# Optimization experiments

Hardware: AMD Instinct MI355X
Metric: run time of the kernel (lower is better)

The kernel has to match this reference:

```python
import jax, jax.numpy as jnp
import numpy as np

T, B, D, H, E = 16, 4096, 256, 512, 32
EPS = 0.1

def setup_inputs() -> dict:
    key = jax.random.key(0)
    ks = jax.random.split(key, 8)
    return {
        "term_emb": jax.random.normal(ks[0], (T, B, D), dtype=jnp.float32),
        "pred_emb": jax.random.normal(ks[1], (E, B, D), dtype=jnp.float32),
        "inv_pred_emb": jax.random.normal(ks[2], (E, B, D), dtype=jnp.float32),
        "signs": jnp.ones((E,), dtype=jnp.float32),
        "W1": jax.random.normal(ks[3], (D, H), dtype=jnp.float32) * (1.0 / np.sqrt(D)),
        "b1": jnp.zeros((H,), dtype=jnp.float32),
        "W2": jax.random.normal(ks[4], (H, D), dtype=jnp.float32) * (1.0 / np.sqrt(H)),
        "b2": jnp.zeros((D,), dtype=jnp.float32),
        "heads": jax.random.randint(ks[5], (E,), 0, T, dtype=jnp.int64),
        "tails": jax.random.randint(ks[6], (E,), 0, T, dtype=jnp.int64),
    }

def reference(term_emb, pred_emb, inv_pred_emb, signs, W1, b1, W2, b2, heads, tails):
    # gather endpoint embeddings per edge: [E, B, D]
    h = term_emb[heads]
    t = term_emb[tails]
    s = signs[:, None, None]
    # estimate_tail_emb (TransE-style NBP): translate by relation embedding
    msg_to_tail = s * (h + pred_emb)      # message along edge direction
    msg_to_head = s * (t + inv_pred_emb)  # message along inverse direction
    # scatter-add messages into per-term slots (sum aggregation)
    agg = (jax.ops.segment_sum(msg_to_tail, tails, num_segments=T)
           + jax.ops.segment_sum(msg_to_head, heads, num_segments=T))
    agg = agg + EPS * term_emb  # residual with eps
    # 1-layer MLP: Linear -> ReLU -> Linear
    hidden = jax.nn.relu(jnp.einsum('tbd,dh->tbh', agg, W1) + b1)
    out = jnp.einsum('tbh,hd->tbd', hidden, W2) + b2
    return out
```

## Files before the change

kernel.cpp:

```cpp
#include <hip/hip_runtime.h>
#include <hip/hip_bf16.h>
#include <stdint.h>

#define T_DIM 16
#define B_DIM 4096
#define D_DIM 256
#define H_DIM 512
#define E_DIM 32
#define M_DIM (T_DIM * B_DIM)
#define BD_DIM (B_DIM * D_DIM)
#define EPS_F 0.1f

typedef __attribute__((ext_vector_type(8))) short short8;
typedef __attribute__((ext_vector_type(4))) float f32x4;

#define GLOBAL_AS __attribute__((address_space(1)))
#define LDS_AS __attribute__((address_space(3)))

__device__ __forceinline__ uint32_t f2bf_rne(float x) {
  uint32_t u = __float_as_uint(x);
  return (u + 0x7fffu + ((u >> 16) & 1u)) >> 16;
}

__device__ __forceinline__ uint4 pack8(const float* f) {
  uint4 v;
  v.x = f2bf_rne(f[0]) | (f2bf_rne(f[1]) << 16);
  v.y = f2bf_rne(f[2]) | (f2bf_rne(f[3]) << 16);
  v.z = f2bf_rne(f[4]) | (f2bf_rne(f[5]) << 16);
  v.w = f2bf_rne(f[6]) | (f2bf_rne(f[7]) << 16);
  return v;
}

__global__ __launch_bounds__(256) void prep_kernel(
    const float* __restrict__ W1, const float* __restrict__ W2,
    uint16_t* __restrict__ W1T, uint16_t* __restrict__ W2T) {
  int idx = blockIdx.x * 256 + threadIdx.x;
  if (idx < D_DIM * H_DIM) {
    int d = idx / H_DIM, h = idx % H_DIM;
    W1T[h * D_DIM + d] = (uint16_t)f2bf_rne(W1[idx]);
    int h2 = idx / D_DIM, d2 = idx % D_DIM;
    W2T[d2 * H_DIM + h2] = (uint16_t)f2bf_rne(W2[idx]);
  }
}

__global__ __launch_bounds__(256) void agg_kernel(
    const float* __restrict__ term, const float* __restrict__ pred,
    const float* __restrict__ inv, const float* __restrict__ signs,
    const int* __restrict__ heads, const int* __restrict__ tails,
    uint16_t* __restrict__ agg) {
  __shared__ int sh_h[E_DIM], sh_t[E_DIM];
  __shared__ float sh_s[E_DIM];
  if (threadIdx.x < E_DIM) {
    int e = threadIdx.x;
    sh_h[e] = heads[e] & (T_DIM - 1);
    sh_t[e] = tails[e] & (T_DIM - 1);
    sh_s[e] = signs[e];
  }
  __syncthreads();

  const int t = blockIdx.y;
  const int j = (blockIdx.x * 256 + threadIdx.x) * 8;

  float acc[8];
  {
    f32x4 a = *reinterpret_cast<const f32x4*>(term + (size_t)t * BD_DIM + j);
    f32x4 b = *reinterpret_cast<const f32x4*>(term + (size_t)t * BD_DIM + j + 4);
    acc[0] = EPS_F * a[0]; acc[1] = EPS_F * a[1]; acc[2] = EPS_F * a[2]; acc[3] = EPS_F * a[3];
    acc[4] = EPS_F * b[0]; acc[5] = EPS_F * b[1]; acc[6] = EPS_F * b[2]; acc[7] = EPS_F * b[3];
  }

#pragma unroll 1
  for (int e = 0; e < E_DIM; ++e) {
    const float s = sh_s[e];
    if (sh_t[e] == t) {
      const f32x4* p = reinterpret_cast<const f32x4*>(pred + (size_t)e * BD_DIM + j);
      const float* hrow = term + (size_t)sh_h[e] * BD_DIM + j;
      f32x4 p0 = __builtin_nontemporal_load(p);
      f32x4 p1 = __builtin_nontemporal_load(p + 1);
      f32x4 h0 = *reinterpret_cast<const f32x4*>(hrow);
      f32x4 h1 = *reinterpret_cast<const f32x4*>(hrow + 4);
      acc[0] += s * (h0[0] + p0[0]); acc[1] += s * (h0[1] + p0[1]);
      acc[2] += s * (h0[2] + p0[2]); acc[3] += s * (h0[3] + p0[3]);
      acc[4] += s * (h1[0] + p1[0]); acc[5] += s * (h1[1] + p1[1]);
      acc[6] += s * (h1[2] + p1[2]); acc[7] += s * (h1[3] + p1[3]);
    }
    if (sh_h[e] == t) {
      const f32x4* iv = reinterpret_cast<const f32x4*>(inv + (size_t)e * BD_DIM + j);
      const float* trow = term + (size_t)sh_t[e] * BD_DIM + j;
      f32x4 i0 = __builtin_nontemporal_load(iv);
      f32x4 i1 = __builtin_nontemporal_load(iv + 1);
      f32x4 t0 = *reinterpret_cast<const f32x4*>(trow);
      f32x4 t1 = *reinterpret_cast<const f32x4*>(trow + 4);
      acc[0] += s * (t0[0] + i0[0]); acc[1] += s * (t0[1] + i0[1]);
      acc[2] += s * (t0[2] + i0[2]); acc[3] += s * (t0[3] + i0[3]);
      acc[4] += s * (t1[0] + i1[0]); acc[5] += s * (t1[1] + i1[1]);
      acc[6] += s * (t1[2] + i1[2]); acc[7] += s * (t1[3] + i1[3]);
    }
  }
  *reinterpret_cast<uint4*>(agg + (size_t)t * BD_DIM + j) = pack8(acc);
}

template <int M, int N, int K, bool RELU, bool OUT_F32>
__global__ __launch_bounds__(256) void gemm_bt(
    const uint16_t* __restrict__ A, const uint16_t* __restrict__ Bt,
    const float* __restrict__ bias, void* __restrict__ Cout) {
  __shared__ __align__(16) uint16_t As[128 * 32];
  __shared__ __align__(16) uint16_t Bs[128 * 32];

  const int tid = threadIdx.x;
  const int w = tid >> 6;
  const int l = tid & 63;
  const int lane16 = l & 15;
  const int quad = l >> 4;
  const int wm = (w & 1) * 64;
  const int wn = (w >> 1) * 64;
  const int m0 = blockIdx.x * 128;
  const int n0 = blockIdx.y * 128;

  f32x4 acc[4][4];
#pragma unroll
  for (int i = 0; i < 4; ++i)
#pragma unroll
    for (int j = 0; j < 4; ++j) acc[i][j] = (f32x4){0.f, 0.f, 0.f, 0.f};

  const int srow = l >> 2;
  const int scol = (l & 3) * 8;

  for (int k0 = 0; k0 < K; k0 += 32) {
#pragma unroll
    for (int c = 0; c < 2; ++c) {
      const int r = w * 32 + c * 16;
      const uint16_t* ga = A + (size_t)(m0 + r + srow) * K + k0 + scol;
      __builtin_amdgcn_global_load_lds((const GLOBAL_AS uint32_t*)ga,
                                       (LDS_AS uint32_t*)(As + r * 32), 16, 0, 0);
      const uint16_t* gb = Bt + (size_t)(n0 + r + srow) * K + k0 + scol;
      __builtin_amdgcn_global_load_lds((const GLOBAL_AS uint32_t*)gb,
                                       (LDS_AS uint32_t*)(Bs + r * 32), 16, 0, 0);
    }
    __syncthreads();

    short8 af[4], bfr[4];
#pragma unroll
    for (int i = 0; i < 4; ++i)
      af[i] = *reinterpret_cast<const short8*>(As + (wm + i * 16 + lane16) * 32 + quad * 8);
#pragma unroll
    for (int j = 0; j < 4; ++j)
      bfr[j] = *reinterpret_cast<const short8*>(Bs + (wn + j * 16 + lane16) * 32 + quad * 8);
#pragma unroll
    for (int i = 0; i < 4; ++i)
#pragma unroll
      for (int j = 0; j < 4; ++j)
        acc[i][j] = __builtin_amdgcn_mfma_f32_16x16x32_bf16(af[i], bfr[j], acc[i][j], 0, 0, 0);
    __syncthreads();
  }

#pragma unroll
  for (int j = 0; j < 4; ++j) {
    const int col = n0 + wn + j * 16 + lane16;
    const float bv = bias[col];
#pragma unroll
    for (int i = 0; i < 4; ++i) {
#pragma unroll
      for (int r = 0; r < 4; ++r) {
        const int row = m0 + wm + i * 16 + quad * 4 + r;
        float x = acc[i][j][r] + bv;
        if (RELU) x = fmaxf(x, 0.f);
        if (OUT_F32) {
          ((float*)Cout)[(size_t)row * N + col] = x;
        } else {
          ((uint16_t*)Cout)[(size_t)row * N + col] = (uint16_t)f2bf_rne(x);
        }
      }
    }
  }
}

extern "C" void kernel_launch(void* const* d_in, const int* in_sizes, int n_in,
                              void* d_out, int out_size, void* d_ws, size_t ws_size,
                              hipStream_t stream) {
  const float* term  = (const float*)d_in[0];
  const float* pred  = (const float*)d_in[1];
  const float* inv   = (const float*)d_in[2];
  const float* signs = (const float*)d_in[3];
  const float* W1    = (const float*)d_in[4];
  const float* b1    = (const float*)d_in[5];
  const float* W2    = (const float*)d_in[6];
  const float* b2    = (const float*)d_in[7];
  const int* heads   = (const int*)d_in[8];
  const int* tails   = (const int*)d_in[9];

  char* ws = (char*)d_ws;
  uint16_t* W1T    = (uint16_t*)(ws);
  uint16_t* W2T    = (uint16_t*)(ws + 262144);
  uint16_t* agg    = (uint16_t*)(ws + 524288);
  uint16_t* hidden = (uint16_t*)(ws + 524288 + 33554432);

  prep_kernel<<<dim3(512), dim3(256), 0, stream>>>(W1, W2, W1T, W2T);
  agg_kernel<<<dim3(BD_DIM / 8 / 256, T_DIM), dim3(256), 0, stream>>>(
      term, pred, inv, signs, heads, tails, agg);
  gemm_bt<M_DIM, H_DIM, D_DIM, true, false><<<dim3(M_DIM / 128, H_DIM / 128), dim3(256), 0, stream>>>(
      agg, W1T, b1, (void*)hidden);
  gemm_bt<M_DIM, D_DIM, H_DIM, false, true><<<dim3(M_DIM / 128, D_DIM / 128), dim3(256), 0, stream>>>(
      hidden, W2T, b2, d_out);
}
```

Before: 427.4 us.

## Keep weight slice resident in LDS and stream A in 64-wide K chunks

The GEMM kernel is restructured so each block preloads its entire 64 KB slice of the transposed weight matrix into LDS once. It then streams only the activation tile in 64-wide K steps, with two MFMA sub-steps per barrier pair. This is meant to cut repeated weight loads and halve the number of synchronisations per K. The second GEMM now uses 64-column blocks with 32x64 wave tiles, which doubles the block count. The catch is about 80 KB of LDS per block, which limits occupancy, and the weight preload is not overlapped with compute.

```diff
diff --git a/kernel.cpp b/kernel.cpp
--- a/kernel.cpp
+++ b/kernel.cpp
@@ -100,66 +100,88 @@
   *reinterpret_cast<uint4*>(agg + (size_t)t * BD_DIM + j) = pack8(acc);
 }
 
-template <int M, int N, int K, bool RELU, bool OUT_F32>
-__global__ __launch_bounds__(256) void gemm_bt(
+template <int M, int N, int K, int BN, int WM, int WN, bool RELU, bool OUT_F32>
+__global__ __launch_bounds__(256) void gemm_wres(
     const uint16_t* __restrict__ A, const uint16_t* __restrict__ Bt,
     const float* __restrict__ bias, void* __restrict__ Cout) {
-  __shared__ __align__(16) uint16_t As[128 * 32];
-  __shared__ __align__(16) uint16_t Bs[128 * 32];
+  static_assert(BN * K == 32768, "W slice must be exactly 64 KB");
+  static_assert((128 / WM) * (BN / WN) == 4, "4 waves must tile the block");
+  __shared__ __align__(16) uint16_t Ws[BN * K];
+  __shared__ __align__(16) uint16_t As[128 * 64];
+
+  constexpr int MI = WM / 16;
+  constexpr int NJ = WN / 16;
+  constexpr int WGM = 128 / WM;
 
   const int tid = threadIdx.x;
   const int w = tid >> 6;
   const int l = tid & 63;
   const int lane16 = l & 15;
   const int quad = l >> 4;
-  const int wm = (w & 1) * 64;
-  const int wn = (w >> 1) * 64;
+  const int wm = (w % WGM) * WM;
+  const int wn = (w / WGM) * WN;
   const int m0 = blockIdx.x * 128;
-  const int n0 = blockIdx.y * 128;
-
-  f32x4 acc[4][4];
-#pragma unroll
-  for (int i = 0; i < 4; ++i)
-#pragma unroll
-    for (int j = 0; j < 4; ++j) acc[i][j] = (f32x4){0.f, 0.f, 0.f, 0.f};
-
-  const int srow = l >> 2;
-  const int scol = (l & 3) * 8;
-
-  for (int k0 = 0; k0 < K; k0 += 32) {
-#pragma unroll
-    for (int c = 0; c < 2; ++c) {
-      const int r = w * 32 + c * 16;
-      const uint16_t* ga = A + (size_t)(m0 + r + srow) * K + k0 + scol;
+  const int n0 = blockIdx.y * BN;
+
+#pragma unroll
+  for (int p = 0; p < 16; ++p) {
+    const int off = p * 2048 + tid * 8;
+    const int kc = off / (BN * 32);
+    const int rem = off - kc * (BN * 32);
+    const int n = rem >> 5;
+    const int c = rem & 31;
+    const uint16_t* g = Bt + (size_t)(n0 + n) * K + kc * 32 + c;
+    __builtin_amdgcn_global_load_lds((const GLOBAL_AS uint32_t*)g,
+                                     (LDS_AS uint32_t*)(Ws + off), 16, 0, 0);
+  }
+
+  f32x4 acc[MI][NJ];
+#pragma unroll
+  for (int i = 0; i < MI; ++i)
+#pragma unroll
+    for (int j = 0; j < NJ; ++j) acc[i][j] = (f32x4){0.f, 0.f, 0.f, 0.f};
+
+  for (int t = 0; t < K / 64; ++t) {
+#pragma unroll
+    for (int c = 0; c < 4; ++c) {
+      const int off = c * 2048 + tid * 8;
+      const int s = off >> 12;
+      const int row = (off >> 5) & 127;
+      const int cc = off & 31;
+      const uint16_t* ga = A + (size_t)(m0 + row) * K + t * 64 + s * 32 + cc;
       __builtin_amdgcn_global_load_lds((const GLOBAL_AS uint32_t*)ga,
-                                       (LDS_AS uint32_t*)(As + r * 32), 16, 0, 0);
-      const uint16_t* gb = Bt + (size_t)(n0 + r + srow) * K + k0 + scol;
-      __builtin_amdgcn_global_load_lds((const GLOBAL_AS uint32_t*)gb,
-                                       (LDS_AS uint32_t*)(Bs + r * 32), 16, 0, 0);
+                                       (LDS_AS uint32_t*)(As + off), 16, 0, 0);
     }
     __syncthreads();
 
-    short8 af[4], bfr[4];
-#pragma unroll
-    for (int i = 0; i < 4; ++i)
-      af[i] = *reinterpret_cast<const short8*>(As + (wm + i * 16 + lane16) * 32 + quad * 8);
-#pragma unroll
-    for (int j = 0; j < 4; ++j)
-      bfr[j] = *reinterpret_cast<const short8*>(Bs + (wn + j * 16 + lane16) * 32 + quad * 8);
-#pragma unroll
-    for (int i = 0; i < 4; ++i)
-#pragma unroll
-      for (int j = 0; j < 4; ++j)
-        acc[i][j] = __builtin_amdgcn_mfma_f32_16x16x32_bf16(af[i], bfr[j], acc[i][j], 0, 0, 0);
+    short8 af[2][MI], bfr[2][NJ];
+#pragma unroll
+    for (int s = 0; s < 2; ++s) {
+#pragma unroll
+      for (int i = 0; i < MI; ++i)
+        af[s][i] = *reinterpret_cast<const short8*>(
+            As + s * 4096 + (wm + i * 16 + lane16) * 32 + quad * 8);
+#pragma unroll
+      for (int j = 0; j < NJ; ++j)
+        bfr[s][j] = *reinterpret_cast<const short8*>(
+            Ws + (t * 2 + s) * (BN * 32) + (wn + j * 16 + lane16) * 32 + quad * 8);
+    }
+#pragma unroll
+    for (int s = 0; s < 2; ++s)
+#pragma unroll
+      for (int i = 0; i < MI; ++i)
+#pragma unroll
+        for (int j = 0; j < NJ; ++j)
+          acc[i][j] = __builtin_amdgcn_mfma_f32_16x16x32_bf16(af[s][i], bfr[s][j], acc[i][j], 0, 0, 0);
     __syncthreads();
   }
 
 #pragma unroll
-  for (int j = 0; j < 4; ++j) {
+  for (int j = 0; j < NJ; ++j) {
     const int col = n0 + wn + j * 16 + lane16;
     const float bv = bias[col];
 #pragma unroll
-    for (int i = 0; i < 4; ++i) {
+    for (int i = 0; i < MI; ++i) {
 #pragma unroll
       for (int r = 0; r < 4; ++r) {
         const int row = m0 + wm + i * 16 + quad * 4 + r;
@@ -198,8 +220,8 @@
   prep_kernel<<<dim3(512), dim3(256), 0, stream>>>(W1, W2, W1T, W2T);
   agg_kernel<<<dim3(BD_DIM / 8 / 256, T_DIM), dim3(256), 0, stream>>>(
       term, pred, inv, signs, heads, tails, agg);
-  gemm_bt<M_DIM, H_DIM, D_DIM, true, false><<<dim3(M_DIM / 128, H_DIM / 128), dim3(256), 0, stream>>>(
-      agg, W1T, b1, (void*)hidden);
-  gemm_bt<M_DIM, D_DIM, H_DIM, false, true><<<dim3(M_DIM / 128, D_DIM / 128), dim3(256), 0, stream>>>(
-      hidden, W2T, b2, d_out);
-}
+  gemm_wres<M_DIM, H_DIM, D_DIM, 128, 64, 64, true, false>
+      <<<dim3(M_DIM / 128, H_DIM / 128), dim3(256), 0, stream>>>(agg, W1T, b1, (void*)hidden);
+  gemm_wres<M_DIM, D_DIM, H_DIM, 64, 32, 64, false, true>
+      <<<dim3(M_DIM / 128, D_DIM / 64), dim3(256), 0, stream>>>(hidden, W2T, b2, d_out);
+}
```

Result: no change. 430.5 us (+0.7%).

## Fuse both MLP GEMMs per row tile and merge weight prep into agg kernel

Applied to the files above, without the earlier changes.

Replaces the two separate GEMM kernels with one fused kernel. Each block keeps a 128-row tile of the aggregated input in LDS, computes the hidden layer in 32-wide slices with bias and ReLU, stages each slice in LDS as bf16, and accumulates the second GEMM in registers. This avoids writing and re-reading the 64 MB bf16 hidden tensor and removes one launch. The weight transpose and bf16 conversion move into an extra grid row of the aggregation kernel, removing another launch. In exchange the fused kernel has only 512 blocks at one block per CU, uses about 64 KB+ of LDS and large accumulator register arrays, and syncs twice per slice, so latency hiding is limited.

```diff
diff --git a/kernel.cpp b/kernel.cpp
--- a/kernel.cpp
+++ b/kernel.cpp
@@ -11,6 +11,10 @@
 #define BD_DIM (B_DIM * D_DIM)
 #define EPS_F 0.1f
 
+#define NSLICE 16
+#define SH 32
+#define HS_LD 40
+
 typedef __attribute__((ext_vector_type(8))) short short8;
 typedef __attribute__((ext_vector_type(4))) float f32x4;
 
@@ -31,23 +35,21 @@
   return v;
 }
 
-__global__ __launch_bounds__(256) void prep_kernel(
-    const float* __restrict__ W1, const float* __restrict__ W2,
-    uint16_t* __restrict__ W1T, uint16_t* __restrict__ W2T) {
-  int idx = blockIdx.x * 256 + threadIdx.x;
-  if (idx < D_DIM * H_DIM) {
-    int d = idx / H_DIM, h = idx % H_DIM;
-    W1T[h * D_DIM + d] = (uint16_t)f2bf_rne(W1[idx]);
-    int h2 = idx / D_DIM, d2 = idx % D_DIM;
-    W2T[d2 * H_DIM + h2] = (uint16_t)f2bf_rne(W2[idx]);
-  }
-}
-
-__global__ __launch_bounds__(256) void agg_kernel(
+__global__ __launch_bounds__(256) void agg_prep_kernel(
     const float* __restrict__ term, const float* __restrict__ pred,
     const float* __restrict__ inv, const float* __restrict__ signs,
     const int* __restrict__ heads, const int* __restrict__ tails,
-    uint16_t* __restrict__ agg) {
+    const float* __restrict__ W1, const float* __restrict__ W2,
+    uint16_t* __restrict__ agg, uint16_t* __restrict__ W1T, uint16_t* __restrict__ W2T) {
+  if (blockIdx.y == T_DIM) {
+    const int idx = blockIdx.x * 256 + threadIdx.x;
+    const int d = idx >> 9, h = idx & (H_DIM - 1);
+    W1T[h * D_DIM + d] = (uint16_t)f2bf_rne(W1[idx]);
+    const int h2 = idx >> 8, d2 = idx & (D_DIM - 1);
+    W2T[d2 * H_DIM + h2] = (uint16_t)f2bf_rne(W2[idx]);
+    return;
+  }
+
   __shared__ int sh_h[E_DIM], sh_t[E_DIM];
   __shared__ float sh_s[E_DIM];
   if (threadIdx.x < E_DIM) {
@@ -100,76 +102,137 @@
   *reinterpret_cast<uint4*>(agg + (size_t)t * BD_DIM + j) = pack8(acc);
 }
 
-template <int M, int N, int K, bool RELU, bool OUT_F32>
-__global__ __launch_bounds__(256) void gemm_bt(
-    const uint16_t* __restrict__ A, const uint16_t* __restrict__ Bt,
-    const float* __restrict__ bias, void* __restrict__ Cout) {
-  __shared__ __align__(16) uint16_t As[128 * 32];
-  __shared__ __align__(16) uint16_t Bs[128 * 32];
+__global__ __launch_bounds__(256, 1) void mlp_fused(
+    const uint16_t* __restrict__ A,
+    const uint16_t* __restrict__ W1T,
+    const uint16_t* __restrict__ W2T,
+    const float* __restrict__ b1, const float* __restrict__ b2,
+    float* __restrict__ Out) {
+  __shared__ __align__(16) uint16_t As[128 * 256];
+  __shared__ __align__(16) uint16_t Wb[2][SH * 256];
+  __shared__ __align__(16) uint16_t Hs[128 * HS_LD];
 
   const int tid = threadIdx.x;
   const int w = tid >> 6;
   const int l = tid & 63;
   const int lane16 = l & 15;
   const int quad = l >> 4;
-  const int wm = (w & 1) * 64;
-  const int wn = (w >> 1) * 64;
   const int m0 = blockIdx.x * 128;
-  const int n0 = blockIdx.y * 128;
-
-  f32x4 acc[4][4];
+
+  const int wm  = (w & 1) * 64;
+  const int wnA = (w >> 1) * 16;
+  const int wn2 = (w >> 1) * 128;
+
+#pragma unroll
+  for (int p = 0; p < 16; ++p) {
+    const int off = p * 2048 + tid * 8;
+    const int kc = off >> 12;
+    const int row = (off >> 5) & 127;
+    const int c = off & 31;
+    const uint16_t* g = A + (size_t)(m0 + row) * D_DIM + kc * 32 + c;
+    __builtin_amdgcn_global_load_lds((const GLOBAL_AS uint32_t*)g,
+                                     (LDS_AS uint32_t*)(As + off), 16, 0, 0);
+  }
+#pragma unroll
+  for (int p = 0; p < 4; ++p) {
+    const int off = p * 2048 + tid * 8;
+    const int kc = off >> 10;
+    const int hl = (off >> 5) & 31;
+    const int c = off & 31;
+    const uint16_t* g = W1T + (size_t)hl * D_DIM + kc * 32 + c;
+    __builtin_amdgcn_global_load_lds((const GLOBAL_AS uint32_t*)g,
+                                     (LDS_AS uint32_t*)(Wb[0] + off), 16, 0, 0);
+  }
+  __syncthreads();
+
+  f32x4 oacc[4][8];
 #pragma unroll
   for (int i = 0; i < 4; ++i)
 #pragma unroll
-    for (int j = 0; j < 4; ++j) acc[i][j] = (f32x4){0.f, 0.f, 0.f, 0.f};
-
-  const int srow = l >> 2;
-  const int scol = (l & 3) * 8;
-
-  for (int k0 = 0; k0 < K; k0 += 32) {
-#pragma unroll
-    for (int c = 0; c < 2; ++c) {
-      const int r = w * 32 + c * 16;
-      const uint16_t* ga = A + (size_t)(m0 + r + srow) * K + k0 + scol;
-      __builtin_amdgcn_global_load_lds((const GLOBAL_AS uint32_t*)ga,
-                                       (LDS_AS uint32_t*)(As + r * 32), 16, 0, 0);
-      const uint16_t* gb = Bt + (size_t)(n0 + r + srow) * K + k0 + scol;
-      __builtin_amdgcn_global_load_lds((const GLOBAL_AS uint32_t*)gb,
-                                       (LDS_AS uint32_t*)(Bs + r * 32), 16, 0, 0);
+    for (int j = 0; j < 8; ++j) oacc[i][j] = (f32x4){0.f, 0.f, 0.f, 0.f};
+
+  for (int s = 0; s < NSLICE; ++s) {
+#pragma unroll
+    for (int p = 0; p < 4; ++p) {
+      const int off = p * 2048 + tid * 8;
+      const int d = off >> 5;
+      const int c = off & 31;
+      const uint16_t* g = W2T + (size_t)d * H_DIM + s * SH + c;
+      __builtin_amdgcn_global_load_lds((const GLOBAL_AS uint32_t*)g,
+                                       (LDS_AS uint32_t*)(Wb[1] + off), 16, 0, 0);
+    }
+
+    f32x4 hacc[4];
+#pragma unroll
+    for (int i = 0; i < 4; ++i) hacc[i] = (f32x4){0.f, 0.f, 0.f, 0.f};
+
+#pragma unroll
+    for (int kk = 0; kk < 8; ++kk) {
+      short8 af[4], bfr;
+      bfr = *reinterpret_cast<const short8*>(Wb[0] + kk * 1024 + (wnA + lane16) * 32 + quad * 8);
+#pragma unroll
+      for (int i = 0; i < 4; ++i)
+        af[i] = *reinterpret_cast<const short8*>(As + kk * 4096 + (wm + i * 16 + lane16) * 32 + quad * 8);
+#pragma unroll
+      for (int i = 0; i < 4; ++i)
+        hacc[i] = __builtin_amdgcn_mfma_f32_16x16x32_bf16(af[i], bfr, hacc[i], 0, 0, 0);
+    }
+
+    {
+      const int hloc = wnA + lane16;
+      const float bv = b1[s * SH + hloc];
+#pragma unroll
+      for (int i = 0; i < 4; ++i) {
+#pragma unroll
+        for (int r = 0; r < 4; ++r) {
+          const int row = wm + i * 16 + quad * 4 + r;
+          const float x = fmaxf(hacc[i][r] + bv, 0.f);
+          Hs[row * HS_LD + hloc] = (uint16_t)f2bf_rne(x);
+        }
+      }
     }
     __syncthreads();
 
-    short8 af[4], bfr[4];
-#pragma unroll
-    for (int i = 0; i < 4; ++i)
-      af[i] = *reinterpret_cast<const short8*>(As + (wm + i * 16 + lane16) * 32 + quad * 8);
-#pragma unroll
-    for (int j = 0; j < 4; ++j)
-      bfr[j] = *reinterpret_cast<const short8*>(Bs + (wn + j * 16 + lane16) * 32 + quad * 8);
-#pragma unroll
-    for (int i = 0; i < 4; ++i)
-#pragma unroll
-      for (int j = 0; j < 4; ++j)
-        acc[i][j] = __builtin_amdgcn_mfma_f32_16x16x32_bf16(af[i], bfr[j], acc[i][j], 0, 0, 0);
+    if (s < NSLICE - 1) {
+#pragma unroll
+      for (int p = 0; p < 4; ++p) {
+        const int off = p * 2048 + tid * 8;
+        const int kc = off >> 10;
+        const int hl = (off >> 5) & 31;
+        const int c = off & 31;
+        const uint16_t* g = W1T + (size_t)((s + 1) * SH + hl) * D_DIM + kc * 32 + c;
+        __builtin_amdgcn_global_load_lds((const GLOBAL_AS uint32_t*)g,
+                                         (LDS_AS uint32_t*)(Wb[0] + off), 16, 0, 0);
+      }
+    }
+
+    {
+      short8 af2[4], bf2[8];
+#pragma unroll
+      for (int i = 0; i < 4; ++i)
+        af2[i] = *reinterpret_cast<const short8*>(Hs + (wm + i * 16 + lane16) * HS_LD + quad * 8);
+#pragma unroll
+      for (int j = 0; j < 8; ++j)
+        bf2[j] = *reinterpret_cast<const short8*>(Wb[1] + (wn2 + j * 16 + lane16) * 32 + quad * 8);
+#pragma unroll
+      for (int i = 0; i < 4; ++i)
+#pragma unroll
+        for (int j = 0; j < 8; ++j)
+          oacc[i][j] = __builtin_amdgcn_mfma_f32_16x16x32_bf16(af2[i], bf2[j], oacc[i][j], 0, 0, 0);
+    }
     __syncthreads();
   }
 
 #pragma unroll
-  for (int j = 0; j < 4; ++j) {
-    const int col = n0 + wn + j * 16 + lane16;
-    const float bv = bias[col];
+  for (int j = 0; j < 8; ++j) {
+    const int col = wn2 + j * 16 + lane16;
+    const float bv = b2[col];
 #pragma unroll
     for (int i = 0; i < 4; ++i) {
 #pragma unroll
       for (int r = 0; r < 4; ++r) {
         const int row = m0 + wm + i * 16 + quad * 4 + r;
-        float x = acc[i][j][r] + bv;
-        if (RELU) x = fmaxf(x, 0.f);
-        if (OUT_F32) {
-          ((float*)Cout)[(size_t)row * N + col] = x;
-        } else {
-          ((uint16_t*)Cout)[(size_t)row * N + col] = (uint16_t)f2bf_rne(x);
-        }
+        Out[(size_t)row * D_DIM + col] = oacc[i][j][r] + bv;
       }
     }
   }
@@ -190,16 +253,12 @@
   const int* tails   = (const int*)d_in[9];
 
   char* ws = (char*)d_ws;
-  uint16_t* W1T    = (uint16_t*)(ws);
-  uint16_t* W2T    = (uint16_t*)(ws + 262144);
-  uint16_t* agg    = (uint16_t*)(ws + 524288);
-  uint16_t* hidden = (uint16_t*)(ws + 524288 + 33554432);
-
-  prep_kernel<<<dim3(512), dim3(256), 0, stream>>>(W1, W2, W1T, W2T);
-  agg_kernel<<<dim3(BD_DIM / 8 / 256, T_DIM), dim3(256), 0, stream>>>(
-      term, pred, inv, signs, heads, tails, agg);
-  gemm_bt<M_DIM, H_DIM, D_DIM, true, false><<<dim3(M_DIM / 128, H_DIM / 128), dim3(256), 0, stream>>>(
-      agg, W1T, b1, (void*)hidden);
-  gemm_bt<M_DIM, D_DIM, H_DIM, false, true><<<dim3(M_DIM / 128, D_DIM / 128), dim3(256), 0, stream>>>(
-      hidden, W2T, b2, d_out);
-}
+  uint16_t* W1T = (uint16_t*)(ws);
+  uint16_t* W2T = (uint16_t*)(ws + 262144);
+  uint16_t* agg = (uint16_t*)(ws + 524288);
+
+  agg_prep_kernel<<<dim3(BD_DIM / 8 / 256, T_DIM + 1), dim3(256), 0, stream>>>(
+      term, pred, inv, signs, heads, tails, W1, W2, agg, W1T, W2T);
+  mlp_fused<<<dim3(M_DIM / 128), dim3(256), 0, stream>>>(
+      agg, W1T, W2T, b1, b2, (float*)d_out);
+}
```

Result: no change. 429.0 us (+0.4%).
